# Performance work log

Measured on AMD Instinct MI355X. Metric: run time of the kernel, lower is better.

The kernel has to match this reference:

```python
import jax, jax.numpy as jnp
import numpy as np
from jax import lax

B, C, H, W = 4, 128, 64, 64
D = C // 2          # VSSBlock hidden_dim
DI = 2 * D          # SS2D d_inner (expand=2)
N = 16              # d_state
R = max(D // 16, 1) # dt_rank
K = 4               # scan directions

def dwconv(x, w, b):
    y = lax.conv_general_dilated(x, w, (1, 1), [(1, 1), (1, 1)],
        dimension_numbers=('NCHW', 'OIHW', 'NCHW'), feature_group_count=x.shape[1])
    return y + b[None, :, None, None]

def layer_norm(x, g, b, eps=1e-5):
    mu = jnp.mean(x, axis=-1, keepdims=True)
    var = jnp.var(x, axis=-1, keepdims=True)
    return (x - mu) * lax.rsqrt(var + eps) * g + b

def selective_scan(u, delta, A, Bs, Cs, Dp):
    # u, delta: (B,K,DI,L); Bs, Cs: (B,K,N,L); A: (K,DI,N); Dp: (K,DI)
    uT = jnp.moveaxis(u, -1, 0)
    dT = jnp.moveaxis(delta, -1, 0)
    BT = jnp.moveaxis(Bs, -1, 0)
    CT = jnp.moveaxis(Cs, -1, 0)
    h0 = jnp.zeros(u.shape[:3] + (A.shape[-1],), u.dtype)
    def step(h, inp):
        u_t, d_t, B_t, C_t = inp
        dA = jnp.exp(d_t[..., None] * A)                       # (B,K,DI,N)
        h = dA * h + (d_t * u_t)[..., None] * B_t[:, :, None, :]
        return h, jnp.einsum('bkdn,bkn->bkd', h, C_t)
    _, ys = lax.scan(step, h0, (uT, dT, BT, CT))
    return jnp.moveaxis(ys, 0, -1) + Dp[None, :, :, None] * u  # (B,K,DI,L)

def ss2d(x, in_proj_w, conv_w, conv_b, x_proj_w, dt_w, dt_b, A_logs, Ds, on_g, on_b, out_proj_w):
    # x: (B,H,W,D)
    b, h, w, _ = x.shape
    L = h * w
    xz = x @ in_proj_w.T                                       # (B,H,W,2*DI)
    xc, z = jnp.split(xz, 2, axis=-1)
    xc = jnp.transpose(xc, (0, 3, 1, 2))                       # (B,DI,H,W)
    xc = jax.nn.silu(dwconv(xc, conv_w, conv_b))
    x1 = xc.reshape(b, DI, L)                                  # row-major scan
    x2 = jnp.transpose(xc, (0, 1, 3, 2)).reshape(b, DI, L)     # col-major scan
    xs = jnp.stack([x1, x2, x1[:, :, ::-1], x2[:, :, ::-1]], axis=1)  # (B,K,DI,L)
    x_dbl = jnp.einsum('bkdl,kcd->bkcl', xs, x_proj_w)
    dts, Bsx, Csx = jnp.split(x_dbl, [R, R + N], axis=2)
    delta = jax.nn.softplus(jnp.einsum('bkrl,kdr->bkdl', dts, dt_w) + dt_b[None, :, :, None])
    A = -jnp.exp(A_logs).reshape(K, DI, N)
    out_y = selective_scan(xs, delta, A, Bsx, Csx, Ds.reshape(K, DI))  # (B,K,DI,L)
    inv_y = out_y[:, 2:4, :, ::-1]
    wh_y = jnp.transpose(out_y[:, 1].reshape(b, DI, w, h), (0, 1, 3, 2)).reshape(b, DI, L)
    invwh_y = jnp.transpose(inv_y[:, 1].reshape(b, DI, w, h), (0, 1, 3, 2)).reshape(b, DI, L)
    y = out_y[:, 0] + inv_y[:, 0] + wh_y + invwh_y             # (B,DI,L)
    y = jnp.transpose(y, (0, 2, 1)).reshape(b, h, w, DI)
    y = layer_norm(y, on_g, on_b) * jax.nn.silu(z)
    return y @ out_proj_w.T                                    # (B,H,W,D)

def _forward(x, dw_w, dw_b, scale, ln1_g, ln1_b, in_proj_w, conv_w, conv_b, x_proj_w, dt_w, dt_b, A_logs, Ds, out_norm_g, out_norm_b, out_proj_w, in_gamma, in_beta):
    xd = dwconv(x, dw_w, dw_b)
    x_1, x_2 = jnp.split(xd, 2, axis=1)
    def branch(xi):
        xp = jnp.transpose(xi, (0, 2, 3, 1))                   # (B,H,W,D)
        y = xp + ss2d(layer_norm(xp, ln1_g, ln1_b), in_proj_w, conv_w, conv_b,
                      x_proj_w, dt_w, dt_b, A_logs, Ds, out_norm_g, out_norm_b, out_proj_w)
        return scale * xi + jnp.transpose(y, (0, 3, 1, 2))
    xo = jnp.concatenate([branch(x_1), branch(x_2)], axis=1)
    mu = jnp.mean(xo, axis=(2, 3), keepdims=True)              # InstanceNorm2d(affine)
    var = jnp.var(xo, axis=(2, 3), keepdims=True)
    xo = (xo - mu) * lax.rsqrt(var + 1e-5) * in_gamma[None, :, None, None] + in_beta[None, :, None, None]
    return jnp.where(xo > 0, xo, 0.01 * xo)                    # LeakyReLU(0.01)

def setup_inputs():
    ks = jax.random.split(jax.random.key(0), 12)
    f = lambda k, shp, s=0.02: jax.random.normal(k, shp, jnp.float32) * s
    return dict(
        x=jax.random.normal(ks[0], (B, C, H, W), jnp.float32),
        dw_w=f(ks[1], (C, 1, 3, 3), 0.1), dw_b=f(ks[2], (C,), 0.1),
        scale=jnp.ones((1,), jnp.float32),
        ln1_g=jnp.ones((D,), jnp.float32), ln1_b=jnp.zeros((D,), jnp.float32),
        in_proj_w=f(ks[3], (2 * DI, D)),
        conv_w=f(ks[4], (DI, 1, 3, 3), 0.1), conv_b=f(ks[5], (DI,), 0.1),
        x_proj_w=f(ks[6], (K, R + 2 * N, DI)),
        dt_w=f(ks[7], (K, DI, R), 0.1), dt_b=f(ks[8], (K, DI), 0.1),
        A_logs=f(ks[9], (K * DI, N), 0.5), Ds=jnp.ones((K * DI,), jnp.float32),
        out_norm_g=jnp.ones((DI,), jnp.float32), out_norm_b=jnp.zeros((DI,), jnp.float32),
        out_proj_w=f(ks[10], (D, DI)),
        in_gamma=jnp.ones((C,), jnp.float32), in_beta=jnp.zeros((C,), jnp.float32),
    )

def reference(x, dw_w, dw_b, scale, ln1_g, ln1_b, in_proj_w, conv_w, conv_b, x_proj_w, dt_w, dt_b, A_logs, Ds, out_norm_g, out_norm_b, out_proj_w, in_gamma, in_beta):
    return _forward(x, dw_w, dw_b, scale, ln1_g, ln1_b, in_proj_w, conv_w, conv_b, x_proj_w, dt_w, dt_b, A_logs, Ds, out_norm_g, out_norm_b, out_proj_w, in_gamma, in_beta)
```

## Files before the change

### kernel.cpp

```cpp
#include <hip/hip_runtime.h>
#include <hip/hip_bf16.h>


__device__ __forceinline__ float LD(const void* p, size_t i, bool isb) {
  if (isb) {
    unsigned short u = ((const unsigned short*)p)[i];
    return __uint_as_float(((unsigned)u) << 16);
  }
  return ((const float*)p)[i];
}
__device__ __forceinline__ unsigned short f2bf(float f) {
  unsigned u = __float_as_uint(f);
  u = (u + 0x7FFFu + ((u >> 16) & 1u)) >> 16;
  return (unsigned short)u;
}
__device__ __forceinline__ float silu_(float x) { return x / (1.f + __expf(-x)); }
__device__ __forceinline__ float softplus_(float x) {
  return x > 20.f ? x : __logf(1.f + __expf(x));
}
#define EXP2R(x) __builtin_amdgcn_exp2f(x)

__global__ void kdet(const void* x, int* flag) {
  if (threadIdx.x == 0 && blockIdx.x == 0) {
    const unsigned short* xs = (const unsigned short*)x;
// ... 91 lines not shown
  }
  __syncthreads();
  int ty = t >> 4, tx = t & 15;
  float acc[4][4];
#pragma unroll
  for (int i = 0; i < 4; ++i)
#pragma unroll
    for (int j = 0; j < 4; ++j) acc[i][j] = 0.f;
  for (int kk = 0; kk < 64; ++kk) {
    float4 a = *(const float4*)&sA[kk][ty * 4];
    float4 bq = *(const float4*)&sB[kk][tx * 4];
    float aa[4] = {a.x, a.y, a.z, a.w}, bb[4] = {bq.x, bq.y, bq.z, bq.w};
#pragma unroll
    for (int i = 0; i < 4; ++i)
#pragma unroll
      for (int j = 0; j < 4; ++j) acc[i][j] += aa[i] * bb[j];
  }
  int c0 = ct * 64 + tx * 4;
#pragma unroll
  for (int i = 0; i < 4; ++i) {
    size_t row = (size_t)row0 + ty * 4 + i;
    float4 o;
    if (c0 < 128) {
      o.x = acc[i][0]; o.y = acc[i][1]; o.z = acc[i][2]; o.w = acc[i][3];
      *(float4*)(T3 + row * 128 + c0) = o;
    } else {
      o.x = silu_(acc[i][0]); o.y = silu_(acc[i][1]); o.z = silu_(acc[i][2]); o.w = silu_(acc[i][3]);
      *(float4*)(T4 + row * 128 + (c0 - 128)) = o;
    }
  }
}

__global__ __launch_bounds__(256) void k3_conv2(
    const float* __restrict__ T3, const void* cw, const void* cb, const void* Ds,
    const int* __restrict__ flag,
    float* __restrict__ U0, float* __restrict__ Ysum)
{
  bool isb = (*flag != 0);
  int e = blockIdx.x >> 6, h = blockIdx.x & 63, dc = blockIdx.y;
  int t = threadIdx.x;
  __shared__ float sI[3][66][65];
  for (int idx = t; idx < 3 * 2 * 64; idx += 256) {
    int r = idx / 128, rem = idx % 128, side = rem >> 6, d = rem & 63;
    sI[r][side * 65][d] = 0.f;
  }
  for (int idx = t; idx < 3 * 64 * 64; idx += 256) {
    int r = idx >> 12, rem = idx & 4095, w = rem >> 6, d = rem & 63;
    int hh = h + r - 1;
    float v = 0.f;
    if (hh >= 0 && hh < 64) v = T3[((size_t)e * 4096 + hh * 64 + w) * 128 + dc * 64 + d];
    sI[r][1 + w][d] = v;
  }
  __syncthreads();
  int d = t & 63, wq = t >> 6;
  int c2 = dc * 64 + d;
  float wt[9];
#pragma unroll
  for (int m = 0; m < 9; ++m) wt[m] = LD(cw, c2 * 9 + m, isb);
  float bias = LD(cb, c2, isb);
  float sd = LD(Ds, c2, isb) + LD(Ds, 128 + c2, isb) + LD(Ds, 256 + c2, isb) + LD(Ds, 384 + c2, isb);
  size_t eb = (size_t)e * 4096;
#pragma unroll
  for (int i = 0; i < 16; ++i) {
    int w = wq * 16 + i;
    float s = bias;
#pragma unroll
    for (int kh = 0; kh < 3; ++kh)
#pragma unroll
      for (int kw = 0; kw < 3; ++kw)
        s += wt[kh * 3 + kw] * sI[kh][w + kw][d];
    s = silu_(s);
    U0[(eb + h * 64 + w) * 128 + c2] = s;
    Ysum[(eb + h * 64 + w) * 128 + c2] = sd * s;
  }
}

__global__ __launch_bounds__(256) void k5_xdbl(
    const float* __restrict__ U0,
    const void* xpw, const int* __restrict__ flag,
    float* __restrict__ dts4, float* __restrict__ Bb2, float* __restrict__ Cb2)
{
  bool isb = (*flag != 0);
  int lt = blockIdx.x;
  int ek = blockIdx.y;
  int e = ek >> 2, k = ek & 3;
  int ls0 = lt * 64;
  int t = threadIdx.x;
  __shared__ float sU[64][132];
  __shared__ float sW[36][132];
  for (int idx = t; idx < 36 * 128; idx += 256) {
    int c = idx >> 7, d = idx & 127;
    sW[c][d] = LD(xpw, ((size_t)k * 36 + c) * 128 + d, isb);
  }
  const bool rev = (k >= 2);
  const int trq = (k & 1);
  for (int idx = t; idx < 2048; idx += 256) {
    int l = idx >> 5, d4 = (idx & 31) * 4;
    int p = rev ? (4095 - ls0 - l) : (ls0 + l);
    int row = trq ? (((p & 63) << 6) | (p >> 6)) : p;
    float4 v = *(const float4*)(U0 + ((size_t)e * 4096 + row) * 128 + d4);
    *(float4*)&sU[l][d4] = v;
  }
  __syncthreads();
  int l = t & 63, cg = t >> 6;
  float acc[9];
#pragma unroll
  for (int j = 0; j < 9; ++j) acc[j] = 0.f;
  for (int dd = 0; dd < 32; ++dd) {
    float4 u4 = *(const float4*)&sU[l][dd * 4];
    float ua[4] = {u4.x, u4.y, u4.z, u4.w};
#pragma unroll
    for (int j = 0; j < 9; ++j) {
      float4 w4 = *(const float4*)&sW[cg * 9 + j][dd * 4];
      acc[j] += ua[0] * w4.x + ua[1] * w4.y + ua[2] * w4.z + ua[3] * w4.w;
    }
  }
  size_t row = (size_t)ek * 4096 + ls0 + l;
  if (cg == 0) {
    float4 o; o.x = acc[0]; o.y = acc[1]; o.z = acc[2]; o.w = acc[3];
    *(float4*)(dts4 + row * 4) = o;
#pragma unroll
    for (int j = 4; j < 9; ++j) Bb2[row * 16 + (j - 4)] = acc[j];
  } else {
#pragma unroll
    for (int j = 0; j < 9; ++j) {
      int c = cg * 9 + j;
      if (c < 20) Bb2[row * 16 + (c - 4)] = acc[j];
      else Cb2[row * 16 + (c - 20)] = acc[j];
    }
  }
}

template<int NSTEPS>
__global__ __launch_bounds__(128) void k6a_chunk(
    const float* __restrict__ U0,
    const float* __restrict__ dts4, const float* __restrict__ Bb2,
    const void* alog, const void* dtw, const void* dtb, const int* __restrict__ flag,
    float* __restrict__ Hs)
{
  bool isb = (*flag != 0);
  int chunk = blockIdx.x, ek = blockIdx.y;
  int e = ek >> 2, k = ek & 3;
  int d = threadIdx.x;
  int ls0 = chunk * NSTEPS;
  float a2[16];
#pragma unroll
  for (int n = 0; n < 16; ++n)
    a2[n] = -__expf(LD(alog, ((size_t)k * 128 + d) * 16 + n, isb)) * 1.44269504f;
  float w0 = LD(dtw, ((size_t)k * 128 + d) * 4 + 0, isb);
  float w1 = LD(dtw, ((size_t)k * 128 + d) * 4 + 1, isb);
  float w2 = LD(dtw, ((size_t)k * 128 + d) * 4 + 2, isb);
  float w3 = LD(dtw, ((size_t)k * 128 + d) * 4 + 3, isb);
  float bd = LD(dtb, k * 128 + d, isb);
  float h[16];
#pragma unroll
  for (int n = 0; n < 16; ++n) h[n] = 0.f;
  float sdelta = 0.f;
  const bool rv = (k >= 2);
  const int tq = (k & 1);
  const float* ubase = U0 + (size_t)e * 4096 * 128 + d;
  const float4* sbase = (const float4*)(dts4 + ((size_t)ek * 4096 + ls0) * 4);
  const float4* bbase = (const float4*)(Bb2 + ((size_t)ek * 4096 + ls0) * 16);
#pragma unroll 2
  for (int s = 0; s < NSTEPS; ++s) {
    float4 s4 = sbase[s];
    float xv = bd + w0 * s4.x + w1 * s4.y + w2 * s4.z + w3 * s4.w;
    float dlt = softplus_(xv);
    int p = ls0 + s;
    int r0 = rv ? (4095 - p) : p;
    int row = tq ? (((r0 & 63) << 6) | (r0 >> 6)) : r0;
    float uu = ubase[(size_t)row * 128];
    float du = dlt * uu;
    float4 b0 = bbase[s * 4 + 0], b1 = bbase[s * 4 + 1], b2 = bbase[s * 4 + 2], b3 = bbase[s * 4 + 3];
    float bb[16] = {b0.x,b0.y,b0.z,b0.w, b1.x,b1.y,b1.z,b1.w,
                    b2.x,b2.y,b2.z,b2.w, b3.x,b3.y,b3.z,b3.w};
    sdelta += dlt;
#pragma unroll
    for (int n = 0; n < 16; ++n) {
      float dA = EXP2R(dlt * a2[n]);
      h[n] = fmaf(dA, h[n], du * bb[n]);
    }
  }
  float2* hp = (float2*)Hs + ((size_t)chunk * 65536 + ek * 2048 + d * 16);
#pragma unroll
  for (int n = 0; n < 16; ++n) {
    float2 o; o.x = h[n]; o.y = EXP2R(a2[n] * sdelta);
    hp[n] = o;
  }
}

__global__ __launch_bounds__(256) void k6b_carry(
    float* __restrict__ Hs, int nchunks)
{
  int idx = blockIdx.x * 256 + threadIdx.x;
  float2* hs = (float2*)Hs;
  float carry = 0.f;
  for (int c0 = 0; c0 < nchunks; c0 += 8) {
    float2 v[8];
#pragma unroll
    for (int j = 0; j < 8; ++j) v[j] = hs[(size_t)(c0 + j) * 65536 + idx];
#pragma unroll
    for (int j = 0; j < 8; ++j) {
      Hs[((size_t)(c0 + j) * 65536 + idx) * 2] = carry;
      carry = v[j].x + v[j].y * carry;
    }
  }
}

template<int NSTEPS>
__global__ __launch_bounds__(128) void k6c_apply(
    const float* __restrict__ U0,
    float* __restrict__ Ysum, const float* __restrict__ dts4,
    const float* __restrict__ Bb2, const float* __restrict__ Cb2,
    const void* alog, const void* dtw, const void* dtb,
    const float* __restrict__ Hs, const int* __restrict__ flag)
{
  bool isb = (*flag != 0);
  int chunk = blockIdx.x, ek = blockIdx.y;
  int e = ek >> 2, k = ek & 3;
  int d = threadIdx.x;
  int ls0 = chunk * NSTEPS;
  float a2[16];
#pragma unroll
  for (int n = 0; n < 16; ++n)
    a2[n] = -__expf(LD(alog, ((size_t)k * 128 + d) * 16 + n, isb)) * 1.44269504f;
  float w0 = LD(dtw, ((size_t)k * 128 + d) * 4 + 0, isb);
  float w1 = LD(dtw, ((size_t)k * 128 + d) * 4 + 1, isb);
  float w2 = LD(dtw, ((size_t)k * 128 + d) * 4 + 2, isb);
  float w3 = LD(dtw, ((size_t)k * 128 + d) * 4 + 3, isb);
  float bd = LD(dtb, k * 128 + d, isb);
  float h[16];
  const float* hp = Hs + ((size_t)chunk * 65536 + ek * 2048 + d * 16) * 2;
#pragma unroll
  for (int n = 0; n < 16; ++n) h[n] = hp[2 * n];
  const bool rv = (k >= 2);
  const int tq = (k & 1);
  const float* ubase = U0 + (size_t)e * 4096 * 128 + d;
  float* ybase = Ysum + (size_t)e * 4096 * 128 + d;
  const float4* sbase = (const float4*)(dts4 + ((size_t)ek * 4096 + ls0) * 4);
  const float4* bbase = (const float4*)(Bb2 + ((size_t)ek * 4096 + ls0) * 16);
  const float4* cbase = (const float4*)(Cb2 + ((size_t)ek * 4096 + ls0) * 16);
#pragma unroll 2
  for (int s = 0; s < NSTEPS; ++s) {
    float4 s4 = sbase[s];
    float xv = bd + w0 * s4.x + w1 * s4.y + w2 * s4.z + w3 * s4.w;
    float dlt = softplus_(xv);
    int p = ls0 + s;
    int r0 = rv ? (4095 - p) : p;
    int row = tq ? (((r0 & 63) << 6) | (r0 >> 6)) : r0;
    float uu = ubase[(size_t)row * 128];
    float du = dlt * uu;
    float4 b0 = bbase[s * 4 + 0], b1 = bbase[s * 4 + 1], b2 = bbase[s * 4 + 2], b3 = bbase[s * 4 + 3];
    float4 c0 = cbase[s * 4 + 0], c1 = cbase[s * 4 + 1], c2 = cbase[s * 4 + 2], c3 = cbase[s * 4 + 3];
    float bb[16] = {b0.x,b0.y,b0.z,b0.w, b1.x,b1.y,b1.z,b1.w,
                    b2.x,b2.y,b2.z,b2.w, b3.x,b3.y,b3.z,b3.w};
    float cc[16] = {c0.x,c0.y,c0.z,c0.w, c1.x,c1.y,c1.z,c1.w,
                    c2.x,c2.y,c2.z,c2.w, c3.x,c3.y,c3.z,c3.w};
    float ya = 0.f, yb = 0.f, yc = 0.f, yd = 0.f;
#pragma unroll
    for (int n = 0; n < 16; n += 4) {
      float dA0 = EXP2R(dlt * a2[n]);
      float dA1 = EXP2R(dlt * a2[n+1]);
      float dA2 = EXP2R(dlt * a2[n+2]);
      float dA3 = EXP2R(dlt * a2[n+3]);
      h[n]   = fmaf(dA0, h[n],   du * bb[n]);
      h[n+1] = fmaf(dA1, h[n+1], du * bb[n+1]);
      h[n+2] = fmaf(dA2, h[n+2], du * bb[n+2]);
      h[n+3] = fmaf(dA3, h[n+3], du * bb[n+3]);
      ya = fmaf(h[n],   cc[n],   ya);
      yb = fmaf(h[n+1], cc[n+1], yb);
      yc = fmaf(h[n+2], cc[n+2], yc);
      yd = fmaf(h[n+3], cc[n+3], yd);
    }
    atomicAdd(ybase + (size_t)row * 128, (ya + yb) + (yc + yd));
  }
}

__global__ __launch_bounds__(256) void k7b_out(
    const float* __restrict__ Ysum, const float* __restrict__ T4,
    const float* __restrict__ T1,
    const void* ong, const void* onb, const void* opw, const void* scale_p,
    const int* __restrict__ flag,
    float* __restrict__ P)
{
  bool isb = (*flag != 0);
  int bid = blockIdx.x; int e = bid >> 7, lt = bid & 127;
  int l0 = lt * 32;
  int t = threadIdx.x;
  __shared__ float sY[32][132];
  __shared__ float sWo[64][132];
  __shared__ float sMu[32], sRs[32];
  __shared__ float sPs[32][8], sPq[32][8];
  __shared__ float sP[64][33];
  for (int idx = t; idx < 8192; idx += 256) sWo[idx >> 7][idx & 127] = LD(opw, idx, isb);
  for (int q = t; q < 1024; q += 256) {
    int l = q >> 5, d4 = (q & 31) * 4;
    float4 v = *(const float4*)(Ysum + ((size_t)e * 4096 + l0 + l) * 128 + d4);
    *(float4*)&sY[l][d4] = v;
  }
  __syncthreads();
  {
    int l = t & 31, g = t >> 5;
    float s = 0.f, q2 = 0.f;
#pragma unroll
    for (int j = 0; j < 16; ++j) { float v = sY[l][g * 16 + j]; s += v; q2 += v * v; }
    sPs[l][g] = s; sPq[l][g] = q2;
  }
  __syncthreads();
  if (t < 32) {
    float s = 0.f, q2 = 0.f;
#pragma unroll
    for (int g = 0; g < 8; ++g) { s += sPs[t][g]; q2 += sPq[t][g]; }
    float mu = s * (1.f / 128.f);
    float var = q2 * (1.f / 128.f) - mu * mu;
    sMu[t] = mu; sRs[t] = rsqrtf(var + 1e-5f);
  }
  __syncthreads();
  for (int idx = t; idx < 4096; idx += 256) {
    int l = idx >> 7, dd2 = idx & 127;
    float v = (sY[l][dd2] - sMu[l]) * sRs[l] * LD(ong, dd2, isb) + LD(onb, dd2, isb);
    v *= T4[((size_t)e * 4096 + l0 + l) * 128 + dd2];
    sY[l][dd2] = v;
  }
  __syncthreads();
  float ops = 1.f + LD(scale_p, 0, isb);
  {
    int l = t & 31, cg = t >> 5;
    float acc[8];
#pragma unroll
    for (int j = 0; j < 8; ++j) acc[j] = 0.f;
// ... 63 lines not shown
    } else {
      float* op = (float*)out + obase;
      float4 o; o.x = o0; o.y = o1; o.z = o2; o.w = o3;
      *(float4*)(op + q * 4) = o;
    }
  }
}

extern "C" void kernel_launch(void* const* d_in, const int* in_sizes, int n_in,
                              void* d_out, int out_size, void* d_ws, size_t ws_size,
                              hipStream_t stream) {
  (void)in_sizes; (void)n_in; (void)out_size; (void)ws_size;
  const void* x      = d_in[0];
  const void* dw_w   = d_in[1];
  const void* dw_b   = d_in[2];
  const void* scale  = d_in[3];
  const void* ln1_g  = d_in[4];
  const void* ln1_b  = d_in[5];
  const void* ipw    = d_in[6];
  const void* conv_w = d_in[7];
  const void* conv_b = d_in[8];
  const void* xpw    = d_in[9];
  const void* dtw    = d_in[10];
  const void* dtb    = d_in[11];
  const void* alog   = d_in[12];
  const void* Ds     = d_in[13];
  const void* ong    = d_in[14];
  const void* onb    = d_in[15];
  const void* opw    = d_in[16];
  const void* ing    = d_in[17];
  const void* inb    = d_in[18];

  float* ws = (float*)d_ws;
  float* T1  = ws;
  float* T2  = ws + 2097152;
  float* T3  = ws + 4194304;
  float* T4  = ws + 8388608;
  float* U0  = ws + 12582912;
  float* Hs  = ws + 16777216;
  float* Ysum = ws + 33554432;
  float* Bb2 = T3;
  float* Cb2 = T3 + 2097152;
  float* dts4 = T2;
  int* flag = (int*)(ws + 37748736);

  hipLaunchKernelGGL(kdet, dim3(1), dim3(64), 0, stream, x, flag);
  hipLaunchKernelGGL(k0_conv_ln, dim3(512), dim3(256), 0, stream, x, dw_w, dw_b, ln1_g, ln1_b, flag, T1, T2);
  hipLaunchKernelGGL(k2_inproj, dim3(512, 4), dim3(256), 0, stream, T2, ipw, flag, T3, T4);
  hipLaunchKernelGGL(k3_conv2, dim3(512, 2), dim3(256), 0, stream, T3, conv_w, conv_b, Ds, flag, U0, Ysum);
  hipLaunchKernelGGL(k5_xdbl, dim3(64, 32), dim3(256), 0, stream, U0, xpw, flag, dts4, Bb2, Cb2);
  hipLaunchKernelGGL(k6a_chunk<32>, dim3(128, 32), dim3(128), 0, stream, U0, dts4, Bb2, alog, dtw, dtb, flag, Hs);
  hipLaunchKernelGGL(k6b_carry, dim3(256), dim3(256), 0, stream, Hs, 128);
  hipLaunchKernelGGL(k6c_apply<32>, dim3(128, 32), dim3(128), 0, stream, U0, Ysum, dts4, Bb2, Cb2, alog, dtw, dtb, Hs, flag);
  hipLaunchKernelGGL(k7b_out, dim3(1024), dim3(256), 0, stream, Ysum, T4, T1, ong, onb, opw, scale, flag, T2);
  hipLaunchKernelGGL(k7c_final, dim3(512), dim3(256), 0, stream, T2, ing, inb, flag, d_out);
}
```

Before: 465.7 us.

## Pair forward/reverse scan directions per block and replace atomics with shared accumulation

The chunked selective scan now processes a forward direction and its reversed counterpart in one block. Both touch the same spatial rows within a chunk, so their outputs are accumulated in shared memory and written once with plain stores instead of per-step global atomicAdds. Row-major and column-major results go to separate buffers that the output kernel sums, and the D-skip term moves from the conv kernel into the apply kernel. The carry pass now stores chunk delta sums rather than decay factors and recomputes the exponentials itself. This costs more registers per thread, half as many blocks, and an extra transposed read in the output kernel.

```diff
diff --git a/kernel.cpp b/kernel.cpp
--- a/kernel.cpp
+++ b/kernel.cpp
@@ -147,9 +147,9 @@
 }
 
 __global__ __launch_bounds__(256) void k3_conv2(
-    const float* __restrict__ T3, const void* cw, const void* cb, const void* Ds,
+    const float* __restrict__ T3, const void* cw, const void* cb,
     const int* __restrict__ flag,
-    float* __restrict__ U0, float* __restrict__ Ysum)
+    float* __restrict__ U0)
 {
   bool isb = (*flag != 0);
   int e = blockIdx.x >> 6, h = blockIdx.x & 63, dc = blockIdx.y;
@@ -173,7 +173,6 @@
 #pragma unroll
   for (int m = 0; m < 9; ++m) wt[m] = LD(cw, c2 * 9 + m, isb);
   float bias = LD(cb, c2, isb);
-  float sd = LD(Ds, c2, isb) + LD(Ds, 128 + c2, isb) + LD(Ds, 256 + c2, isb) + LD(Ds, 384 + c2, isb);
   size_t eb = (size_t)e * 4096;
 #pragma unroll
   for (int i = 0; i < 16; ++i) {
@@ -186,7 +185,6 @@
         s += wt[kh * 3 + kw] * sI[kh][w + kw][d];
     s = silu_(s);
     U0[(eb + h * 64 + w) * 128 + c2] = s;
-    Ysum[(eb + h * 64 + w) * 128 + c2] = sd * s;
   }
 }
 
@@ -251,73 +249,105 @@
     const float* __restrict__ U0,
     const float* __restrict__ dts4, const float* __restrict__ Bb2,
     const void* alog, const void* dtw, const void* dtb, const int* __restrict__ flag,
-    float* __restrict__ Hs)
-{
-  bool isb = (*flag != 0);
-  int chunk = blockIdx.x, ek = blockIdx.y;
-  int e = ek >> 2, k = ek & 3;
+    float* __restrict__ Hsh, float* __restrict__ Sdl)
+{
+  constexpr int NCH = 4096 / NSTEPS;
+  bool isb = (*flag != 0);
+  int c = blockIdx.x;
+  int e = blockIdx.y >> 1, pa = blockIdx.y & 1;
   int d = threadIdx.x;
-  int ls0 = chunk * NSTEPS;
-  float a2[16];
-#pragma unroll
-  for (int n = 0; n < 16; ++n)
-    a2[n] = -__expf(LD(alog, ((size_t)k * 128 + d) * 16 + n, isb)) * 1.44269504f;
-  float w0 = LD(dtw, ((size_t)k * 128 + d) * 4 + 0, isb);
-  float w1 = LD(dtw, ((size_t)k * 128 + d) * 4 + 1, isb);
-  float w2 = LD(dtw, ((size_t)k * 128 + d) * 4 + 2, isb);
-  float w3 = LD(dtw, ((size_t)k * 128 + d) * 4 + 3, isb);
-  float bd = LD(dtb, k * 128 + d, isb);
-  float h[16];
-#pragma unroll
-  for (int n = 0; n < 16; ++n) h[n] = 0.f;
-  float sdelta = 0.f;
-  const bool rv = (k >= 2);
-  const int tq = (k & 1);
+  int kA = pa, kB = pa + 2;
+  int ekA = e * 4 + kA, ekB = e * 4 + kB;
+  int cB = (NCH - 1) - c;
+  int r0 = c * NSTEPS;
+  float a2A[16], a2B[16];
+#pragma unroll
+  for (int n = 0; n < 16; ++n) {
+    a2A[n] = -__expf(LD(alog, ((size_t)kA * 128 + d) * 16 + n, isb)) * 1.44269504f;
+    a2B[n] = -__expf(LD(alog, ((size_t)kB * 128 + d) * 16 + n, isb)) * 1.44269504f;
+  }
+  float wA0 = LD(dtw, ((size_t)kA * 128 + d) * 4 + 0, isb);
+  float wA1 = LD(dtw, ((size_t)kA * 128 + d) * 4 + 1, isb);
+  float wA2 = LD(dtw, ((size_t)kA * 128 + d) * 4 + 2, isb);
+  float wA3 = LD(dtw, ((size_t)kA * 128 + d) * 4 + 3, isb);
+  float bdA = LD(dtb, kA * 128 + d, isb);
+  float wB0 = LD(dtw, ((size_t)kB * 128 + d) * 4 + 0, isb);
+  float wB1 = LD(dtw, ((size_t)kB * 128 + d) * 4 + 1, isb);
+  float wB2 = LD(dtw, ((size_t)kB * 128 + d) * 4 + 2, isb);
+  float wB3 = LD(dtw, ((size_t)kB * 128 + d) * 4 + 3, isb);
+  float bdB = LD(dtb, kB * 128 + d, isb);
+  float hA[16], hB[16];
+#pragma unroll
+  for (int n = 0; n < 16; ++n) { hA[n] = 0.f; hB[n] = 0.f; }
+  float sdA = 0.f, sdB = 0.f;
   const float* ubase = U0 + (size_t)e * 4096 * 128 + d;
-  const float4* sbase = (const float4*)(dts4 + ((size_t)ek * 4096 + ls0) * 4);
-  const float4* bbase = (const float4*)(Bb2 + ((size_t)ek * 4096 + ls0) * 16);
+  const float4* sbA = (const float4*)(dts4 + ((size_t)ekA * 4096 + (size_t)c * NSTEPS) * 4);
+  const float4* sbB = (const float4*)(dts4 + ((size_t)ekB * 4096 + (size_t)cB * NSTEPS) * 4);
+  const float4* bbA = (const float4*)(Bb2 + ((size_t)ekA * 4096 + (size_t)c * NSTEPS) * 16);
+  const float4* bbB = (const float4*)(Bb2 + ((size_t)ekB * 4096 + (size_t)cB * NSTEPS) * 16);
 #pragma unroll 2
   for (int s = 0; s < NSTEPS; ++s) {
-    float4 s4 = sbase[s];
-    float xv = bd + w0 * s4.x + w1 * s4.y + w2 * s4.z + w3 * s4.w;
-    float dlt = softplus_(xv);
-    int p = ls0 + s;
-    int r0 = rv ? (4095 - p) : p;
-    int row = tq ? (((r0 & 63) << 6) | (r0 >> 6)) : r0;
-    float uu = ubase[(size_t)row * 128];
-    float du = dlt * uu;
-    float4 b0 = bbase[s * 4 + 0], b1 = bbase[s * 4 + 1], b2 = bbase[s * 4 + 2], b3 = bbase[s * 4 + 3];
-    float bb[16] = {b0.x,b0.y,b0.z,b0.w, b1.x,b1.y,b1.z,b1.w,
-                    b2.x,b2.y,b2.z,b2.w, b3.x,b3.y,b3.z,b3.w};
-    sdelta += dlt;
-#pragma unroll
-    for (int n = 0; n < 16; ++n) {
-      float dA = EXP2R(dlt * a2[n]);
-      h[n] = fmaf(dA, h[n], du * bb[n]);
-    }
-  }
-  float2* hp = (float2*)Hs + ((size_t)chunk * 65536 + ek * 2048 + d * 16);
-#pragma unroll
-  for (int n = 0; n < 16; ++n) {
-    float2 o; o.x = h[n]; o.y = EXP2R(a2[n] * sdelta);
-    hp[n] = o;
-  }
+    float4 s4A = sbA[s], s4B = sbB[s];
+    float dltA = softplus_(bdA + wA0 * s4A.x + wA1 * s4A.y + wA2 * s4A.z + wA3 * s4A.w);
+    float dltB = softplus_(bdB + wB0 * s4B.x + wB1 * s4B.y + wB2 * s4B.z + wB3 * s4B.w);
+    int qA = r0 + s, qB = r0 + (NSTEPS - 1) - s;
+    int rowA = pa ? (((qA & 63) << 6) | (qA >> 6)) : qA;
+    int rowB = pa ? (((qB & 63) << 6) | (qB >> 6)) : qB;
+    float duA = dltA * ubase[(size_t)rowA * 128];
+    float duB = dltB * ubase[(size_t)rowB * 128];
+    sdA += dltA; sdB += dltB;
+#pragma unroll
+    for (int n4 = 0; n4 < 4; ++n4) {
+      float4 b4A = bbA[s * 4 + n4];
+      hA[n4*4+0] = fmaf(EXP2R(dltA * a2A[n4*4+0]), hA[n4*4+0], duA * b4A.x);
+      hA[n4*4+1] = fmaf(EXP2R(dltA * a2A[n4*4+1]), hA[n4*4+1], duA * b4A.y);
+      hA[n4*4+2] = fmaf(EXP2R(dltA * a2A[n4*4+2]), hA[n4*4+2], duA * b4A.z);
+      hA[n4*4+3] = fmaf(EXP2R(dltA * a2A[n4*4+3]), hA[n4*4+3], duA * b4A.w);
+      float4 b4B = bbB[s * 4 + n4];
+      hB[n4*4+0] = fmaf(EXP2R(dltB * a2B[n4*4+0]), hB[n4*4+0], duB * b4B.x);
+      hB[n4*4+1] = fmaf(EXP2R(dltB * a2B[n4*4+1]), hB[n4*4+1], duB * b4B.y);
+      hB[n4*4+2] = fmaf(EXP2R(dltB * a2B[n4*4+2]), hB[n4*4+2], duB * b4B.z);
+      hB[n4*4+3] = fmaf(EXP2R(dltB * a2B[n4*4+3]), hB[n4*4+3], duB * b4B.w);
+    }
+  }
+  float* hpA = Hsh + (size_t)c * 65536 + (size_t)ekA * 2048 + (size_t)d * 16;
+  float* hpB = Hsh + (size_t)cB * 65536 + (size_t)ekB * 2048 + (size_t)d * 16;
+#pragma unroll
+  for (int n4 = 0; n4 < 4; ++n4) {
+    float4 oA; oA.x = hA[n4*4]; oA.y = hA[n4*4+1]; oA.z = hA[n4*4+2]; oA.w = hA[n4*4+3];
+    *(float4*)(hpA + n4 * 4) = oA;
+    float4 oB; oB.x = hB[n4*4]; oB.y = hB[n4*4+1]; oB.z = hB[n4*4+2]; oB.w = hB[n4*4+3];
+    *(float4*)(hpB + n4 * 4) = oB;
+  }
+  Sdl[(size_t)c * 4096 + ekA * 128 + d] = sdA;
+  Sdl[(size_t)cB * 4096 + ekB * 128 + d] = sdB;
 }
 
 __global__ __launch_bounds__(256) void k6b_carry(
-    float* __restrict__ Hs, int nchunks)
-{
+    const float* __restrict__ Hsh, const float* __restrict__ Sdl,
+    const void* alog, const int* __restrict__ flag,
+    float* __restrict__ Carry)
+{
+  bool isb = (*flag != 0);
   int idx = blockIdx.x * 256 + threadIdx.x;
-  float2* hs = (float2*)Hs;
+  int ek = idx >> 11, rem = idx & 2047, d = rem >> 4, n = rem & 15;
+  int k = ek & 3;
+  float a2 = -__expf(LD(alog, ((size_t)k * 128 + d) * 16 + n, isb)) * 1.44269504f;
+  int sidx = ek * 128 + d;
   float carry = 0.f;
-  for (int c0 = 0; c0 < nchunks; c0 += 8) {
-    float2 v[8];
-#pragma unroll
-    for (int j = 0; j < 8; ++j) v[j] = hs[(size_t)(c0 + j) * 65536 + idx];
+  for (int c0 = 0; c0 < 128; c0 += 8) {
+    float hv[8], pA[8];
 #pragma unroll
     for (int j = 0; j < 8; ++j) {
-      Hs[((size_t)(c0 + j) * 65536 + idx) * 2] = carry;
-      carry = v[j].x + v[j].y * carry;
+      hv[j] = Hsh[(size_t)(c0 + j) * 65536 + idx];
+      pA[j] = Sdl[(size_t)(c0 + j) * 4096 + sidx];
+    }
+#pragma unroll
+    for (int j = 0; j < 8; ++j) pA[j] = EXP2R(a2 * pA[j]);
+#pragma unroll
+    for (int j = 0; j < 8; ++j) {
+      Carry[(size_t)(c0 + j) * 65536 + idx] = carry;
+      carry = fmaf(pA[j], carry, hv[j]);
     }
   }
 }
@@ -325,75 +355,108 @@
 template<int NSTEPS>
 __global__ __launch_bounds__(128) void k6c_apply(
     const float* __restrict__ U0,
-    float* __restrict__ Ysum, const float* __restrict__ dts4,
+    float* __restrict__ Ysum, float* __restrict__ YsT,
+    const float* __restrict__ dts4,
     const float* __restrict__ Bb2, const float* __restrict__ Cb2,
-    const void* alog, const void* dtw, const void* dtb,
-    const float* __restrict__ Hs, const int* __restrict__ flag)
-{
-  bool isb = (*flag != 0);
-  int chunk = blockIdx.x, ek = blockIdx.y;
-  int e = ek >> 2, k = ek & 3;
+    const void* alog, const void* dtw, const void* dtb, const void* Ds,
+    const float* __restrict__ Carry, const int* __restrict__ flag)
+{
+  constexpr int NCH = 4096 / NSTEPS;
+  bool isb = (*flag != 0);
+  int c = blockIdx.x;
+  int e = blockIdx.y >> 1, pa = blockIdx.y & 1;
   int d = threadIdx.x;
-  int ls0 = chunk * NSTEPS;
-  float a2[16];
-#pragma unroll
-  for (int n = 0; n < 16; ++n)
-    a2[n] = -__expf(LD(alog, ((size_t)k * 128 + d) * 16 + n, isb)) * 1.44269504f;
-  float w0 = LD(dtw, ((size_t)k * 128 + d) * 4 + 0, isb);
-  float w1 = LD(dtw, ((size_t)k * 128 + d) * 4 + 1, isb);
-  float w2 = LD(dtw, ((size_t)k * 128 + d) * 4 + 2, isb);
-  float w3 = LD(dtw, ((size_t)k * 128 + d) * 4 + 3, isb);
-  float bd = LD(dtb, k * 128 + d, isb);
-  float h[16];
-  const float* hp = Hs + ((size_t)chunk * 65536 + ek * 2048 + d * 16) * 2;
-#pragma unroll
-  for (int n = 0; n < 16; ++n) h[n] = hp[2 * n];
-  const bool rv = (k >= 2);
-  const int tq = (k & 1);
+  int kA = pa, kB = pa + 2;
+  int ekA = e * 4 + kA, ekB = e * 4 + kB;
+  int cB = (NCH - 1) - c;
+  int r0 = c * NSTEPS;
+  __shared__ float sY[NSTEPS][128];
+#pragma unroll
+  for (int r = 0; r < NSTEPS; ++r) sY[r][d] = 0.f;
+  float a2A[16], a2B[16];
+#pragma unroll
+  for (int n = 0; n < 16; ++n) {
+    a2A[n] = -__expf(LD(alog, ((size_t)kA * 128 + d) * 16 + n, isb)) * 1.44269504f;
+    a2B[n] = -__expf(LD(alog, ((size_t)kB * 128 + d) * 16 + n, isb)) * 1.44269504f;
+  }
+  float wA0 = LD(dtw, ((size_t)kA * 128 + d) * 4 + 0, isb);
+  float wA1 = LD(dtw, ((size_t)kA * 128 + d) * 4 + 1, isb);
+  float wA2 = LD(dtw, ((size_t)kA * 128 + d) * 4 + 2, isb);
+  float wA3 = LD(dtw, ((size_t)kA * 128 + d) * 4 + 3, isb);
+  float bdA = LD(dtb, kA * 128 + d, isb);
+  float wB0 = LD(dtw, ((size_t)kB * 128 + d) * 4 + 0, isb);
+  float wB1 = LD(dtw, ((size_t)kB * 128 + d) * 4 + 1, isb);
+  float wB2 = LD(dtw, ((size_t)kB * 128 + d) * 4 + 2, isb);
+  float wB3 = LD(dtw, ((size_t)kB * 128 + d) * 4 + 3, isb);
+  float bdB = LD(dtb, kB * 128 + d, isb);
+  float sd = 0.f;
+  if (pa == 0)
+    sd = LD(Ds, d, isb) + LD(Ds, 128 + d, isb) + LD(Ds, 256 + d, isb) + LD(Ds, 384 + d, isb);
+  float hA[16], hB[16];
+  {
+    const float* cpA = Carry + (size_t)c * 65536 + (size_t)ekA * 2048 + (size_t)d * 16;
+    const float* cpB = Carry + (size_t)cB * 65536 + (size_t)ekB * 2048 + (size_t)d * 16;
+#pragma unroll
+    for (int n = 0; n < 16; ++n) { hA[n] = cpA[n]; hB[n] = cpB[n]; }
+  }
   const float* ubase = U0 + (size_t)e * 4096 * 128 + d;
-  float* ybase = Ysum + (size_t)e * 4096 * 128 + d;
-  const float4* sbase = (const float4*)(dts4 + ((size_t)ek * 4096 + ls0) * 4);
-  const float4* bbase = (const float4*)(Bb2 + ((size_t)ek * 4096 + ls0) * 16);
-  const float4* cbase = (const float4*)(Cb2 + ((size_t)ek * 4096 + ls0) * 16);
+  const float4* sbA = (const float4*)(dts4 + ((size_t)ekA * 4096 + (size_t)c * NSTEPS) * 4);
+  const float4* sbB = (const float4*)(dts4 + ((size_t)ekB * 4096 + (size_t)cB * NSTEPS) * 4);
+  const float4* bbA = (const float4*)(Bb2 + ((size_t)ekA * 4096 + (size_t)c * NSTEPS) * 16);
+  const float4* bbB = (const float4*)(Bb2 + ((size_t)ekB * 4096 + (size_t)cB * NSTEPS) * 16);
+  const float4* cbA = (const float4*)(Cb2 + ((size_t)ekA * 4096 + (size_t)c * NSTEPS) * 16);
+  const float4* cbB = (const float4*)(Cb2 + ((size_t)ekB * 4096 + (size_t)cB * NSTEPS) * 16);
 #pragma unroll 2
   for (int s = 0; s < NSTEPS; ++s) {
-    float4 s4 = sbase[s];
-    float xv = bd + w0 * s4.x + w1 * s4.y + w2 * s4.z + w3 * s4.w;
-    float dlt = softplus_(xv);
-    int p = ls0 + s;
-    int r0 = rv ? (4095 - p) : p;
-    int row = tq ? (((r0 & 63) << 6) | (r0 >> 6)) : r0;
-    float uu = ubase[(size_t)row * 128];
-    float du = dlt * uu;
-    float4 b0 = bbase[s * 4 + 0], b1 = bbase[s * 4 + 1], b2 = bbase[s * 4 + 2], b3 = bbase[s * 4 + 3];
-    float4 c0 = cbase[s * 4 + 0], c1 = cbase[s * 4 + 1], c2 = cbase[s * 4 + 2], c3 = cbase[s * 4 + 3];
-    float bb[16] = {b0.x,b0.y,b0.z,b0.w, b1.x,b1.y,b1.z,b1.w,
-                    b2.x,b2.y,b2.z,b2.w, b3.x,b3.y,b3.z,b3.w};
-    float cc[16] = {c0.x,c0.y,c0.z,c0.w, c1.x,c1.y,c1.z,c1.w,
-                    c2.x,c2.y,c2.z,c2.w, c3.x,c3.y,c3.z,c3.w};
-    float ya = 0.f, yb = 0.f, yc = 0.f, yd = 0.f;
-#pragma unroll
-    for (int n = 0; n < 16; n += 4) {
-      float dA0 = EXP2R(dlt * a2[n]);
-      float dA1 = EXP2R(dlt * a2[n+1]);
-      float dA2 = EXP2R(dlt * a2[n+2]);
-      float dA3 = EXP2R(dlt * a2[n+3]);
-      h[n]   = fmaf(dA0, h[n],   du * bb[n]);
-      h[n+1] = fmaf(dA1, h[n+1], du * bb[n+1]);
-      h[n+2] = fmaf(dA2, h[n+2], du * bb[n+2]);
-      h[n+3] = fmaf(dA3, h[n+3], du * bb[n+3]);
-      ya = fmaf(h[n],   cc[n],   ya);
-      yb = fmaf(h[n+1], cc[n+1], yb);
-      yc = fmaf(h[n+2], cc[n+2], yc);
-      yd = fmaf(h[n+3], cc[n+3], yd);
-    }
-    atomicAdd(ybase + (size_t)row * 128, (ya + yb) + (yc + yd));
+    float4 s4A = sbA[s], s4B = sbB[s];
+    float dltA = softplus_(bdA + wA0 * s4A.x + wA1 * s4A.y + wA2 * s4A.z + wA3 * s4A.w);
+    float dltB = softplus_(bdB + wB0 * s4B.x + wB1 * s4B.y + wB2 * s4B.z + wB3 * s4B.w);
+    int qA = r0 + s, qB = r0 + (NSTEPS - 1) - s;
+    int rowA = pa ? (((qA & 63) << 6) | (qA >> 6)) : qA;
+    int rowB = pa ? (((qB & 63) << 6) | (qB >> 6)) : qB;
+    float uuA = ubase[(size_t)rowA * 128];
+    float uuB = ubase[(size_t)rowB * 128];
+    float duA = dltA * uuA, duB = dltB * uuB;
+    float yA = 0.f, yB = 0.f;
+#pragma unroll
+    for (int n4 = 0; n4 < 4; ++n4) {
+      float4 b4A = bbA[s * 4 + n4];
+      float4 c4A = cbA[s * 4 + n4];
+      hA[n4*4+0] = fmaf(EXP2R(dltA * a2A[n4*4+0]), hA[n4*4+0], duA * b4A.x);
+      hA[n4*4+1] = fmaf(EXP2R(dltA * a2A[n4*4+1]), hA[n4*4+1], duA * b4A.y);
+      hA[n4*4+2] = fmaf(EXP2R(dltA * a2A[n4*4+2]), hA[n4*4+2], duA * b4A.z);
+      hA[n4*4+3] = fmaf(EXP2R(dltA * a2A[n4*4+3]), hA[n4*4+3], duA * b4A.w);
+      yA = fmaf(hA[n4*4+0], c4A.x, yA);
+      yA = fmaf(hA[n4*4+1], c4A.y, yA);
+      yA = fmaf(hA[n4*4+2], c4A.z, yA);
+      yA = fmaf(hA[n4*4+3], c4A.w, yA);
+      float4 b4B = bbB[s * 4 + n4];
+      float4 c4B = cbB[s * 4 + n4];
+      hB[n4*4+0] = fmaf(EXP2R(dltB * a2B[n4*4+0]), hB[n4*4+0], duB * b4B.x);
+      hB[n4*4+1] = fmaf(EXP2R(dltB * a2B[n4*4+1]), hB[n4*4+1], duB * b4B.y);
+      hB[n4*4+2] = fmaf(EXP2R(dltB * a2B[n4*4+2]), hB[n4*4+2], duB * b4B.z);
+      hB[n4*4+3] = fmaf(EXP2R(dltB * a2B[n4*4+3]), hB[n4*4+3], duB * b4B.w);
+      yB = fmaf(hB[n4*4+0], c4B.x, yB);
+      yB = fmaf(hB[n4*4+1], c4B.y, yB);
+      yB = fmaf(hB[n4*4+2], c4B.z, yB);
+      yB = fmaf(hB[n4*4+3], c4B.w, yB);
+    }
+    sY[s][d] += fmaf(sd, uuA, yA);
+    sY[NSTEPS - 1 - s][d] += yB;
+  }
+  __syncthreads();
+  float* obase = (pa ? YsT : Ysum) + ((size_t)e * 4096 + r0) * 128;
+  const float* sflat = (const float*)sY;
+#pragma unroll
+  for (int j = 0; j < NSTEPS / 4; ++j) {
+    int off = j * 512 + d * 4;
+    *(float4*)(obase + off) = *(const float4*)(sflat + off);
   }
 }
 
 __global__ __launch_bounds__(256) void k7b_out(
-    const float* __restrict__ Ysum, const float* __restrict__ T4,
-    const float* __restrict__ T1,
+    const float* __restrict__ Ysum, const float* __restrict__ YsT,
+    const float* __restrict__ T4, const float* __restrict__ T1,
     const void* ong, const void* onb, const void* opw, const void* scale_p,
     const int* __restrict__ flag,
     float* __restrict__ P)
@@ -408,9 +471,13 @@
   __shared__ float sPs[32][8], sPq[32][8];
   __shared__ float sP[64][33];
   for (int idx = t; idx < 8192; idx += 256) sWo[idx >> 7][idx & 127] = LD(opw, idx, isb);
+  int hh = l0 >> 6;
+  int w0_ = l0 & 63;
   for (int q = t; q < 1024; q += 256) {
     int l = q >> 5, d4 = (q & 31) * 4;
     float4 v = *(const float4*)(Ysum + ((size_t)e * 4096 + l0 + l) * 128 + d4);
+    float4 v2 = *(const float4*)(YsT + ((size_t)e * 4096 + (w0_ + l) * 64 + hh) * 128 + d4);
+    v.x += v2.x; v.y += v2.y; v.z += v2.z; v.w += v2.w;
     *(float4*)&sY[l][d4] = v;
   }
   __syncthreads();
@@ -540,26 +607,29 @@
   const void* inb    = d_in[18];
 
   float* ws = (float*)d_ws;
-  float* T1  = ws;
-  float* T2  = ws + 2097152;
-  float* T3  = ws + 4194304;
-  float* T4  = ws + 8388608;
-  float* U0  = ws + 12582912;
-  float* Hs  = ws + 16777216;
-  float* Ysum = ws + 33554432;
-  float* Bb2 = T3;
-  float* Cb2 = T3 + 2097152;
+  float* T1   = ws;
+  float* T2   = ws + 2097152;
+  float* T3   = ws + 4194304;
+  float* T4   = ws + 8388608;
+  float* U0   = ws + 12582912;
+  float* Hsh  = ws + 16777216;
+  float* Carry= ws + 25165824;
+  float* Sdl  = ws + 33554432;
+  float* Ysum = ws + 34078720;
+  float* YsT  = ws + 38273024;
+  float* Bb2  = T3;
+  float* Cb2  = T3 + 2097152;
   float* dts4 = T2;
-  int* flag = (int*)(ws + 37748736);
+  int* flag = (int*)(ws + 42467328);
 
   hipLaunchKernelGGL(kdet, dim3(1), dim3(64), 0, stream, x, flag);
   hipLaunchKernelGGL(k0_conv_ln, dim3(512), dim3(256), 0, stream, x, dw_w, dw_b, ln1_g, ln1_b, flag, T1, T2);
   hipLaunchKernelGGL(k2_inproj, dim3(512, 4), dim3(256), 0, stream, T2, ipw, flag, T3, T4);
-  hipLaunchKernelGGL(k3_conv2, dim3(512, 2), dim3(256), 0, stream, T3, conv_w, conv_b, Ds, flag, U0, Ysum);
+  hipLaunchKernelGGL(k3_conv2, dim3(512, 2), dim3(256), 0, stream, T3, conv_w, conv_b, flag, U0);
   hipLaunchKernelGGL(k5_xdbl, dim3(64, 32), dim3(256), 0, stream, U0, xpw, flag, dts4, Bb2, Cb2);
-  hipLaunchKernelGGL(k6a_chunk<32>, dim3(128, 32), dim3(128), 0, stream, U0, dts4, Bb2, alog, dtw, dtb, flag, Hs);
-  hipLaunchKernelGGL(k6b_carry, dim3(256), dim3(256), 0, stream, Hs, 128);
-  hipLaunchKernelGGL(k6c_apply<32>, dim3(128, 32), dim3(128), 0, stream, U0, Ysum, dts4, Bb2, Cb2, alog, dtw, dtb, Hs, flag);
-  hipLaunchKernelGGL(k7b_out, dim3(1024), dim3(256), 0, stream, Ysum, T4, T1, ong, onb, opw, scale, flag, T2);
+  hipLaunchKernelGGL(k6a_chunk<32>, dim3(128, 16), dim3(128), 0, stream, U0, dts4, Bb2, alog, dtw, dtb, flag, Hsh, Sdl);
+  hipLaunchKernelGGL(k6b_carry, dim3(256), dim3(256), 0, stream, Hsh, Sdl, alog, flag, Carry);
+  hipLaunchKernelGGL(k6c_apply<32>, dim3(128, 16), dim3(128), 0, stream, U0, Ysum, YsT, dts4, Bb2, Cb2, alog, dtw, dtb, Ds, Carry, flag);
+  hipLaunchKernelGGL(k7b_out, dim3(1024), dim3(256), 0, stream, Ysum, YsT, T4, T1, ong, onb, opw, scale, flag, T2);
   hipLaunchKernelGGL(k7c_final, dim3(512), dim3(256), 0, stream, T2, ing, inb, flag, d_out);
 }
```

Result: slower. 486.7 us (+4.5%).

## Stage scan B/C/dt in LDS and split chunk state into separate arrays

Applied to the files above, without the earlier changes.

The chunked-scan kernels now copy each chunk's dt, B and C rows into shared memory once per block, instead of having every thread issue the same broadcast global loads. The chunk state buffer changes from interleaved (h, decay) pairs to a contiguous h array plus a per-channel summed delta. The carry kernel recomputes the decay with exp2 and writes into a separate Carry buffer, and the apply kernel reads it contiguously. This trades some extra exp work in the carry pass and a block barrier for less redundant global traffic and fewer bytes written per chunk.

```diff
diff --git a/kernel.cpp b/kernel.cpp
--- a/kernel.cpp
+++ b/kernel.cpp
@@ -251,13 +251,21 @@
     const float* __restrict__ U0,
     const float* __restrict__ dts4, const float* __restrict__ Bb2,
     const void* alog, const void* dtw, const void* dtb, const int* __restrict__ flag,
-    float* __restrict__ Hs)
+    float* __restrict__ Hsh, float* __restrict__ Sdl)
 {
   bool isb = (*flag != 0);
   int chunk = blockIdx.x, ek = blockIdx.y;
   int e = ek >> 2, k = ek & 3;
   int d = threadIdx.x;
   int ls0 = chunk * NSTEPS;
+  __shared__ float4 sDt[NSTEPS];
+  __shared__ float4 sB[NSTEPS * 4];
+  {
+    const float4* srcd = (const float4*)(dts4 + ((size_t)ek * 4096 + ls0) * 4);
+    const float4* srcb = (const float4*)(Bb2 + ((size_t)ek * 4096 + ls0) * 16);
+    if (d < NSTEPS) sDt[d] = srcd[d];
+    sB[d] = srcb[d];
+  }
   float a2[16];
 #pragma unroll
   for (int n = 0; n < 16; ++n)
@@ -274,11 +282,10 @@
   const bool rv = (k >= 2);
   const int tq = (k & 1);
   const float* ubase = U0 + (size_t)e * 4096 * 128 + d;
-  const float4* sbase = (const float4*)(dts4 + ((size_t)ek * 4096 + ls0) * 4);
-  const float4* bbase = (const float4*)(Bb2 + ((size_t)ek * 4096 + ls0) * 16);
+  __syncthreads();
 #pragma unroll 2
   for (int s = 0; s < NSTEPS; ++s) {
-    float4 s4 = sbase[s];
+    float4 s4 = sDt[s];
     float xv = bd + w0 * s4.x + w1 * s4.y + w2 * s4.z + w3 * s4.w;
     float dlt = softplus_(xv);
     int p = ls0 + s;
@@ -286,38 +293,50 @@
     int row = tq ? (((r0 & 63) << 6) | (r0 >> 6)) : r0;
     float uu = ubase[(size_t)row * 128];
     float du = dlt * uu;
-    float4 b0 = bbase[s * 4 + 0], b1 = bbase[s * 4 + 1], b2 = bbase[s * 4 + 2], b3 = bbase[s * 4 + 3];
-    float bb[16] = {b0.x,b0.y,b0.z,b0.w, b1.x,b1.y,b1.z,b1.w,
-                    b2.x,b2.y,b2.z,b2.w, b3.x,b3.y,b3.z,b3.w};
     sdelta += dlt;
 #pragma unroll
-    for (int n = 0; n < 16; ++n) {
-      float dA = EXP2R(dlt * a2[n]);
-      h[n] = fmaf(dA, h[n], du * bb[n]);
-    }
-  }
-  float2* hp = (float2*)Hs + ((size_t)chunk * 65536 + ek * 2048 + d * 16);
-#pragma unroll
-  for (int n = 0; n < 16; ++n) {
-    float2 o; o.x = h[n]; o.y = EXP2R(a2[n] * sdelta);
-    hp[n] = o;
-  }
+    for (int n4 = 0; n4 < 4; ++n4) {
+      float4 b4 = sB[s * 4 + n4];
+      h[n4*4+0] = fmaf(EXP2R(dlt * a2[n4*4+0]), h[n4*4+0], du * b4.x);
+      h[n4*4+1] = fmaf(EXP2R(dlt * a2[n4*4+1]), h[n4*4+1], du * b4.y);
+      h[n4*4+2] = fmaf(EXP2R(dlt * a2[n4*4+2]), h[n4*4+2], du * b4.z);
+      h[n4*4+3] = fmaf(EXP2R(dlt * a2[n4*4+3]), h[n4*4+3], du * b4.w);
+    }
+  }
+  float* hp = Hsh + (size_t)chunk * 65536 + (size_t)ek * 2048 + (size_t)d * 16;
+#pragma unroll
+  for (int n4 = 0; n4 < 4; ++n4) {
+    float4 o; o.x = h[n4*4]; o.y = h[n4*4+1]; o.z = h[n4*4+2]; o.w = h[n4*4+3];
+    *(float4*)(hp + n4 * 4) = o;
+  }
+  Sdl[(size_t)chunk * 4096 + ek * 128 + d] = sdelta;
 }
 
 __global__ __launch_bounds__(256) void k6b_carry(
-    float* __restrict__ Hs, int nchunks)
-{
+    const float* __restrict__ Hsh, const float* __restrict__ Sdl,
+    const void* alog, const int* __restrict__ flag,
+    float* __restrict__ Carry)
+{
+  bool isb = (*flag != 0);
   int idx = blockIdx.x * 256 + threadIdx.x;
-  float2* hs = (float2*)Hs;
+  int ek = idx >> 11, rem = idx & 2047, d = rem >> 4, n = rem & 15;
+  int k = ek & 3;
+  float a2 = -__expf(LD(alog, ((size_t)k * 128 + d) * 16 + n, isb)) * 1.44269504f;
+  int sidx = ek * 128 + d;
   float carry = 0.f;
-  for (int c0 = 0; c0 < nchunks; c0 += 8) {
-    float2 v[8];
-#pragma unroll
-    for (int j = 0; j < 8; ++j) v[j] = hs[(size_t)(c0 + j) * 65536 + idx];
+  for (int c0 = 0; c0 < 128; c0 += 8) {
+    float hv[8], pA[8];
 #pragma unroll
     for (int j = 0; j < 8; ++j) {
-      Hs[((size_t)(c0 + j) * 65536 + idx) * 2] = carry;
-      carry = v[j].x + v[j].y * carry;
+      hv[j] = Hsh[(size_t)(c0 + j) * 65536 + idx];
+      pA[j] = Sdl[(size_t)(c0 + j) * 4096 + sidx];
+    }
+#pragma unroll
+    for (int j = 0; j < 8; ++j) pA[j] = EXP2R(a2 * pA[j]);
+#pragma unroll
+    for (int j = 0; j < 8; ++j) {
+      Carry[(size_t)(c0 + j) * 65536 + idx] = carry;
+      carry = fmaf(pA[j], carry, hv[j]);
     }
   }
 }
@@ -328,13 +347,24 @@
     float* __restrict__ Ysum, const float* __restrict__ dts4,
     const float* __restrict__ Bb2, const float* __restrict__ Cb2,
     const void* alog, const void* dtw, const void* dtb,
-    const float* __restrict__ Hs, const int* __restrict__ flag)
+    const float* __restrict__ Carry, const int* __restrict__ flag)
 {
   bool isb = (*flag != 0);
   int chunk = blockIdx.x, ek = blockIdx.y;
   int e = ek >> 2, k = ek & 3;
   int d = threadIdx.x;
   int ls0 = chunk * NSTEPS;
+  __shared__ float4 sDt[NSTEPS];
+  __shared__ float4 sB[NSTEPS * 4];
+  __shared__ float4 sC[NSTEPS * 4];
+  {
+    const float4* srcd = (const float4*)(dts4 + ((size_t)ek * 4096 + ls0) * 4);
+    const float4* srcb = (const float4*)(Bb2 + ((size_t)ek * 4096 + ls0) * 16);
+    const float4* srcc = (const float4*)(Cb2 + ((size_t)ek * 4096 + ls0) * 16);
+    if (d < NSTEPS) sDt[d] = srcd[d];
+    sB[d] = srcb[d];
+    sC[d] = srcc[d];
+  }
   float a2[16];
 #pragma unroll
   for (int n = 0; n < 16; ++n)
@@ -345,19 +375,19 @@
   float w3 = LD(dtw, ((size_t)k * 128 + d) * 4 + 3, isb);
   float bd = LD(dtb, k * 128 + d, isb);
   float h[16];
-  const float* hp = Hs + ((size_t)chunk * 65536 + ek * 2048 + d * 16) * 2;
-#pragma unroll
-  for (int n = 0; n < 16; ++n) h[n] = hp[2 * n];
+  {
+    const float* cp = Carry + (size_t)chunk * 65536 + (size_t)ek * 2048 + (size_t)d * 16;
+#pragma unroll
+    for (int n = 0; n < 16; ++n) h[n] = cp[n];
+  }
   const bool rv = (k >= 2);
   const int tq = (k & 1);
   const float* ubase = U0 + (size_t)e * 4096 * 128 + d;
   float* ybase = Ysum + (size_t)e * 4096 * 128 + d;
-  const float4* sbase = (const float4*)(dts4 + ((size_t)ek * 4096 + ls0) * 4);
-  const float4* bbase = (const float4*)(Bb2 + ((size_t)ek * 4096 + ls0) * 16);
-  const float4* cbase = (const float4*)(Cb2 + ((size_t)ek * 4096 + ls0) * 16);
+  __syncthreads();
 #pragma unroll 2
   for (int s = 0; s < NSTEPS; ++s) {
-    float4 s4 = sbase[s];
+    float4 s4 = sDt[s];
     float xv = bd + w0 * s4.x + w1 * s4.y + w2 * s4.z + w3 * s4.w;
     float dlt = softplus_(xv);
     int p = ls0 + s;
@@ -365,27 +395,19 @@
     int row = tq ? (((r0 & 63) << 6) | (r0 >> 6)) : r0;
     float uu = ubase[(size_t)row * 128];
     float du = dlt * uu;
-    float4 b0 = bbase[s * 4 + 0], b1 = bbase[s * 4 + 1], b2 = bbase[s * 4 + 2], b3 = bbase[s * 4 + 3];
-    float4 c0 = cbase[s * 4 + 0], c1 = cbase[s * 4 + 1], c2 = cbase[s * 4 + 2], c3 = cbase[s * 4 + 3];
-    float bb[16] = {b0.x,b0.y,b0.z,b0.w, b1.x,b1.y,b1.z,b1.w,
-                    b2.x,b2.y,b2.z,b2.w, b3.x,b3.y,b3.z,b3.w};
-    float cc[16] = {c0.x,c0.y,c0.z,c0.w, c1.x,c1.y,c1.z,c1.w,
-                    c2.x,c2.y,c2.z,c2.w, c3.x,c3.y,c3.z,c3.w};
     float ya = 0.f, yb = 0.f, yc = 0.f, yd = 0.f;
 #pragma unroll
-    for (int n = 0; n < 16; n += 4) {
-      float dA0 = EXP2R(dlt * a2[n]);
-      float dA1 = EXP2R(dlt * a2[n+1]);
-      float dA2 = EXP2R(dlt * a2[n+2]);
-      float dA3 = EXP2R(dlt * a2[n+3]);
-      h[n]   = fmaf(dA0, h[n],   du * bb[n]);
-      h[n+1] = fmaf(dA1, h[n+1], du * bb[n+1]);
-      h[n+2] = fmaf(dA2, h[n+2], du * bb[n+2]);
-      h[n+3] = fmaf(dA3, h[n+3], du * bb[n+3]);
-      ya = fmaf(h[n],   cc[n],   ya);
-      yb = fmaf(h[n+1], cc[n+1], yb);
-      yc = fmaf(h[n+2], cc[n+2], yc);
-      yd = fmaf(h[n+3], cc[n+3], yd);
+    for (int n4 = 0; n4 < 4; ++n4) {
+      float4 b4 = sB[s * 4 + n4];
+      float4 c4 = sC[s * 4 + n4];
+      h[n4*4+0] = fmaf(EXP2R(dlt * a2[n4*4+0]), h[n4*4+0], du * b4.x);
+      h[n4*4+1] = fmaf(EXP2R(dlt * a2[n4*4+1]), h[n4*4+1], du * b4.y);
+      h[n4*4+2] = fmaf(EXP2R(dlt * a2[n4*4+2]), h[n4*4+2], du * b4.z);
+      h[n4*4+3] = fmaf(EXP2R(dlt * a2[n4*4+3]), h[n4*4+3], du * b4.w);
+      ya = fmaf(h[n4*4+0], c4.x, ya);
+      yb = fmaf(h[n4*4+1], c4.y, yb);
+      yc = fmaf(h[n4*4+2], c4.z, yc);
+      yd = fmaf(h[n4*4+3], c4.w, yd);
     }
     atomicAdd(ybase + (size_t)row * 128, (ya + yb) + (yc + yd));
   }
@@ -540,26 +562,28 @@
   const void* inb    = d_in[18];
 
   float* ws = (float*)d_ws;
-  float* T1  = ws;
-  float* T2  = ws + 2097152;
-  float* T3  = ws + 4194304;
-  float* T4  = ws + 8388608;
-  float* U0  = ws + 12582912;
-  float* Hs  = ws + 16777216;
-  float* Ysum = ws + 33554432;
-  float* Bb2 = T3;
-  float* Cb2 = T3 + 2097152;
+  float* T1   = ws;
+  float* T2   = ws + 2097152;
+  float* T3   = ws + 4194304;
+  float* T4   = ws + 8388608;
+  float* U0   = ws + 12582912;
+  float* Hsh  = ws + 16777216;
+  float* Carry= ws + 25165824;
+  float* Sdl  = ws + 33554432;
+  float* Ysum = ws + 34078720;
+  float* Bb2  = T3;
+  float* Cb2  = T3 + 2097152;
   float* dts4 = T2;
-  int* flag = (int*)(ws + 37748736);
+  int* flag = (int*)(ws + 38273024);
 
   hipLaunchKernelGGL(kdet, dim3(1), dim3(64), 0, stream, x, flag);
   hipLaunchKernelGGL(k0_conv_ln, dim3(512), dim3(256), 0, stream, x, dw_w, dw_b, ln1_g, ln1_b, flag, T1, T2);
   hipLaunchKernelGGL(k2_inproj, dim3(512, 4), dim3(256), 0, stream, T2, ipw, flag, T3, T4);
   hipLaunchKernelGGL(k3_conv2, dim3(512, 2), dim3(256), 0, stream, T3, conv_w, conv_b, Ds, flag, U0, Ysum);
   hipLaunchKernelGGL(k5_xdbl, dim3(64, 32), dim3(256), 0, stream, U0, xpw, flag, dts4, Bb2, Cb2);
-  hipLaunchKernelGGL(k6a_chunk<32>, dim3(128, 32), dim3(128), 0, stream, U0, dts4, Bb2, alog, dtw, dtb, flag, Hs);
-  hipLaunchKernelGGL(k6b_carry, dim3(256), dim3(256), 0, stream, Hs, 128);
-  hipLaunchKernelGGL(k6c_apply<32>, dim3(128, 32), dim3(128), 0, stream, U0, Ysum, dts4, Bb2, Cb2, alog, dtw, dtb, Hs, flag);
+  hipLaunchKernelGGL(k6a_chunk<32>, dim3(128, 32), dim3(128), 0, stream, U0, dts4, Bb2, alog, dtw, dtb, flag, Hsh, Sdl);
+  hipLaunchKernelGGL(k6b_carry, dim3(256), dim3(256), 0, stream, Hsh, Sdl, alog, flag, Carry);
+  hipLaunchKernelGGL(k6c_apply<32>, dim3(128, 32), dim3(128), 0, stream, U0, Ysum, dts4, Bb2, Cb2, alog, dtw, dtb, Carry, flag);
   hipLaunchKernelGGL(k7b_out, dim3(1024), dim3(256), 0, stream, Ysum, T4, T1, ong, onb, opw, scale, flag, T2);
   hipLaunchKernelGGL(k7c_final, dim3(512), dim3(256), 0, stream, T2, ing, inb, flag, d_out);
 }
```

Result: faster. 450.0 us (-3.4%).
